# Kernel optimization log

Hardware: AMD Instinct MI355X
Metric: run time of the kernel (lower is better)

The kernel has to match this reference:

```python
import jax, jax.numpy as jnp
import numpy as np

B, S, D = 2, 2048, 1024
H = 16
HD = D // H

def setup_inputs() -> dict:
    key = jax.random.key(0)
    ks = jax.random.split(key, 6)
    sc = 0.02
    return {
        'x': jax.random.normal(ks[0], (B, S, D), jnp.float32),
        'Wq': jax.random.normal(ks[1], (D, D), jnp.float32) * sc,
        'Wk': jax.random.normal(ks[2], (D, D), jnp.float32) * sc,
        'Wv': jax.random.normal(ks[3], (D, D), jnp.float32) * sc,
        'Wo': jax.random.normal(ks[4], (D, D), jnp.float32) * sc,
        'bo': jnp.zeros((D,), jnp.float32),
    }

def reference(x, Wq, Wk, Wv, Wo, bo):
    b, s, d_in = x.shape
    # torch Linear: y = x @ W.T
    q = jnp.einsum('bsd,ed->bse', x, Wq)
    k = jnp.einsum('bsd,ed->bse', x, Wk)
    v = jnp.einsum('bsd,ed->bse', x, Wv)
    # [b, h, s, hd]
    q = q.reshape(b, s, H, HD).transpose(0, 2, 1, 3)
    k = k.reshape(b, s, H, HD).transpose(0, 2, 1, 3)
    v = v.reshape(b, s, H, HD).transpose(0, 2, 1, 3)
    # NOTE: original divides by sqrt(d_out), not sqrt(head_dim)
    scores = jnp.einsum('bhqd,bhkd->bhqk', q, k) / jnp.sqrt(jnp.float32(D))
    causal = jnp.tril(jnp.ones((s, s), dtype=bool))  # True = keep
    scores = jnp.where(causal[None, None], scores, -jnp.inf)
    attn = jax.nn.softmax(scores, axis=-1)
    ctx = jnp.einsum('bhqk,bhkd->bhqd', attn, v)
    ctx = ctx.transpose(0, 2, 1, 3).reshape(b, s, D)
    return jnp.einsum('bsd,ed->bse', ctx, Wo) + bo
```

## Files before the change

### kernel.cpp

```cpp
#include <hip/hip_runtime.h>
#include <hip/hip_bf16.h>
#include <stdint.h>

typedef unsigned short u16;
typedef __attribute__((ext_vector_type(8))) short short8;
typedef __attribute__((ext_vector_type(4))) float f32x4;
typedef __attribute__((ext_vector_type(16))) float f32x16;
typedef __attribute__((ext_vector_type(4))) u16 u16x4;

#define NB 2
#define NS 2048
#define ND 1024
#define NH 16
#define NM 4096

#define QSCALE 0.045084220f

#if __has_builtin(__builtin_amdgcn_exp2f)
#define EXP2(x) __builtin_amdgcn_exp2f(x)
#else
__device__ __forceinline__ float __exp2_asm(float x){
  float r;
  asm("v_exp_f32 %0, %1" : "=v"(r) : "v"(x));
  return r;
}
#define EXP2(x) __exp2_asm(x)
#endif
#if __has_builtin(__builtin_amdgcn_rcpf)
#define RCP(x) __builtin_amdgcn_rcpf(x)
#else
#define RCP(x) (1.0f / (x))
#endif

__device__ __forceinline__ u16 f2bf(float f){
  union { float f; unsigned u; } v; v.f = f;
  unsigned r = v.u + 0x7fff + ((v.u >> 16) & 1);
  return (u16)(r >> 16);
}

__device__ __forceinline__ unsigned cvtpk(float lo, float hi){
  unsigned r;
  asm("v_cvt_pk_bf16_f32 %0, %1, %2" : "=v"(r) : "v"(lo), "v"(hi));
  return r;
}

__device__ __forceinline__ void pl32swap(unsigned &e, unsigned &o){
  asm("v_permlane32_swap_b32 %0, %1" : "+v"(e), "+v"(o));
}

__device__ __forceinline__ void gload_lds16(const u16* g, u16* l){
  __builtin_amdgcn_global_load_lds(
      (const __attribute__((address_space(1))) unsigned int*)g,
      (__attribute__((address_space(3))) unsigned int*)l, 16, 0, 0);
}

__device__ __forceinline__ f32x16 mfma32(short8 a, short8 b, f32x16 c){
  return __builtin_amdgcn_mfma_f32_32x32x16_bf16(a, b, c, 0, 0, 0);
}

__global__ void cvt_all(const float* __restrict__ x,
                        const float* __restrict__ wq, const float* __restrict__ wk,
                        const float* __restrict__ wv, const float* __restrict__ wo,
                        u16* __restrict__ xb, u16* __restrict__ wqb, u16* __restrict__ wkb,
                        u16* __restrict__ wvb, u16* __restrict__ wob){
  int ib = blockIdx.x;
  const float* s; u16* d; int off;
  if (ib < 4096){ s = x; d = xb; off = ib; }
  else {
    int t = ib - 4096, sel = t >> 10;
    off = t & 1023;
    s = (sel == 0) ? wq : (sel == 1) ? wk : (sel == 2) ? wv : wo;
    d = (sel == 0) ? wqb : (sel == 1) ? wkb : (sel == 2) ? wvb : wob;
  }
  int i = (off * 256 + threadIdx.x) * 4;
  float4 v = *(const float4*)(s + i);
  u16x4 pk = { f2bf(v.x), f2bf(v.y), f2bf(v.z), f2bf(v.w) };
  *(u16x4*)(d + i) = pk;
}

__device__ __forceinline__ void gemm_core(
    const u16* __restrict__ A, const u16* __restrict__ W,
    int m0, int n0, u16* lsA, u16* lsB, f32x4 acc[4][4])
{
  const int tid = threadIdx.x;
  const int l   = tid & 63;
  const int wr  = (tid >> 7) & 1;
  const int wc  = (tid >> 6) & 1;
  const int lr  = l & 15;
  const int lkb = (l >> 4) << 4;
  const int sr  = tid >> 3;
  const int scb = (tid & 7) << 4;

  for (int kt = 0; kt < 16; ++kt){
    const int k0 = kt << 6;
    #pragma unroll
    for (int i = 0; i < 4; ++i){
      int r   = (i << 5) + sr;
      int cbs = scb ^ ((r & 7) << 4);
      gload_lds16(&A[(size_t)(m0 + r) * ND + k0 + (cbs >> 1)], &lsA[r * 64 + (scb >> 1)]);
      gload_lds16(&W[(size_t)(n0 + r) * ND + k0 + (cbs >> 1)], &lsB[r * 64 + (scb >> 1)]);
    }
    __syncthreads();

    short8 af[4][2], bf[4][2];
    #pragma unroll
    for (int m16 = 0; m16 < 4; ++m16){
      int r  = (wr << 6) + (m16 << 4) + lr;
      int rx = (r & 7) << 4;
      #pragma unroll
      for (int ks = 0; ks < 2; ++ks){
        int off = r * 128 + (((ks << 6) + lkb) ^ rx);
        af[m16][ks] = *(const short8*)((const char*)lsA + off);
      }
    }
    #pragma unroll
    for (int n16 = 0; n16 < 4; ++n16){
      int r  = (wc << 6) + (n16 << 4) + lr;
      int rx = (r & 7) << 4;
      #pragma unroll
      for (int ks = 0; ks < 2; ++ks){
        int off = r * 128 + (((ks << 6) + lkb) ^ rx);
        bf[n16][ks] = *(const short8*)((const char*)lsB + off);
      }
    }
    #pragma unroll
    for (int m16 = 0; m16 < 4; ++m16)
      #pragma unroll
      for (int n16 = 0; n16 < 4; ++n16){
        acc[m16][n16] = __builtin_amdgcn_mfma_f32_16x16x32_bf16(af[m16][0], bf[n16][0], acc[m16][n16], 0, 0, 0);
        acc[m16][n16] = __builtin_amdgcn_mfma_f32_16x16x32_bf16(af[m16][1], bf[n16][1], acc[m16][n16], 0, 0, 0);
      }
    __syncthreads();
  }
}

__global__ __launch_bounds__(256) void gemm_qkv(
    const u16* __restrict__ xb,
    const u16* __restrict__ Wqb, const u16* __restrict__ Wkb, const u16* __restrict__ Wvb,
    u16* __restrict__ Qo, u16* __restrict__ Ko, u16* __restrict__ Vt)
{
  __shared__ u16 lsA[128*64];
  __shared__ u16 lsB[128*64];
  const int z = blockIdx.z;
  const u16* W = (z == 0) ? Wqb : (z == 1) ? Wkb : Wvb;
  const int m0 = blockIdx.x << 7, n0 = blockIdx.y << 7;
  f32x4 acc[4][4] = {};
  gemm_core(xb, W, m0, n0, lsA, lsB, acc);

  const int l  = threadIdx.x & 63;
  const int wr = (threadIdx.x >> 7) & 1, wc = (threadIdx.x >> 6) & 1;
  const int rb = m0 + (wr << 6) + ((l >> 4) << 2);
  const int cb = n0 + (wc << 6) + (l & 15);

  if (z < 2){
    const float sc = (z == 0) ? QSCALE : 1.0f;
    u16* C = (z == 0) ? Qo : Ko;
    #pragma unroll
    for (int m16 = 0; m16 < 4; ++m16)
      #pragma unroll
      for (int n16 = 0; n16 < 4; ++n16)
        #pragma unroll
        for (int r = 0; r < 4; ++r)
          C[(size_t)(rb + (m16 << 4) + r) * ND + cb + (n16 << 4)] = f2bf(acc[m16][n16][r] * sc);
  } else {
    #pragma unroll
    for (int m16 = 0; m16 < 4; ++m16){
      int srow = rb + (m16 << 4);
      int bi = srow >> 11, s = srow & 2047;
      #pragma unroll
      for (int n16 = 0; n16 < 4; ++n16){
        int col = cb + (n16 << 4);
        u16x4 pk = { f2bf(acc[m16][n16][0]), f2bf(acc[m16][n16][1]),
                     f2bf(acc[m16][n16][2]), f2bf(acc[m16][n16][3]) };
        *(u16x4*)&Vt[((size_t)(bi * 16 + (col >> 6)) * 64 + (col & 63)) * 2048 + s] = pk;
      }
    }
  }
}

__global__ __launch_bounds__(256) void gemm_out(
    const u16* __restrict__ ctxb, const u16* __restrict__ Wob,
    const float* __restrict__ bo, float* __restrict__ out)
{
  __shared__ u16 lsA[64*64];
  __shared__ u16 lsB[128*64];
  const int m0 = blockIdx.x << 6, n0 = blockIdx.y << 7;
  const int tid = threadIdx.x;
  const int l = tid & 63;
  const int w = tid >> 6;
  const int lr = l & 15;
  const int lkb = (l >> 4) << 4;
  const int rl = tid >> 3, ch = tid & 7;

  f32x4 acc[4][2] = {};

  for (int kt = 0; kt < 16; ++kt){
    const int k0 = kt << 6;
    #pragma unroll
    for (int k = 0; k < 2; ++k){
      int rr = rl + (k << 5);
      int cs = ch ^ (rr & 7);
      gload_lds16(&ctxb[(size_t)(m0 + rr) * ND + k0 + cs * 8], &lsA[rr * 64 + ch * 8]);
    }
    #pragma unroll
    for (int k = 0; k < 4; ++k){
      int rr = rl + (k << 5);
      int cs = ch ^ (rr & 7);
      gload_lds16(&Wob[(size_t)(n0 + rr) * ND + k0 + cs * 8], &lsB[rr * 64 + ch * 8]);
    }
    __syncthreads();

    short8 af[4][2], bf[2][2];
    #pragma unroll
    for (int m16 = 0; m16 < 4; ++m16){
      int r  = (m16 << 4) + lr;
      int rx = (r & 7) << 4;
      #pragma unroll
      for (int ks = 0; ks < 2; ++ks)
        af[m16][ks] = *(const short8*)((const char*)lsA + r * 128 + (((ks << 6) + lkb) ^ rx));
    }
    #pragma unroll
    for (int n16 = 0; n16 < 2; ++n16){
      int r  = (w << 5) + (n16 << 4) + lr;
      int rx = (r & 7) << 4;
      #pragma unroll
      for (int ks = 0; ks < 2; ++ks)
        bf[n16][ks] = *(const short8*)((const char*)lsB + r * 128 + (((ks << 6) + lkb) ^ rx));
    }
    #pragma unroll
    for (int m16 = 0; m16 < 4; ++m16)
      #pragma unroll
      for (int n16 = 0; n16 < 2; ++n16){
        acc[m16][n16] = __builtin_amdgcn_mfma_f32_16x16x32_bf16(af[m16][0], bf[n16][0], acc[m16][n16], 0, 0, 0);
        acc[m16][n16] = __builtin_amdgcn_mfma_f32_16x16x32_bf16(af[m16][1], bf[n16][1], acc[m16][n16], 0, 0, 0);
      }
    __syncthreads();
  }

  const int rb = m0 + ((l >> 4) << 2);
  const int cb = n0 + (w << 5) + lr;
  #pragma unroll
  for (int m16 = 0; m16 < 4; ++m16)
    #pragma unroll
    for (int n16 = 0; n16 < 2; ++n16)
      #pragma unroll
      for (int r = 0; r < 4; ++r){
        int col = cb + (n16 << 4);
        out[(size_t)(rb + (m16 << 4) + r) * ND + col] = acc[m16][n16][r] + bo[col];
      }
}

__device__ __forceinline__ void stage_tile(const u16* src, int srcStride, u16* lds, int tid){
  const int rl = tid >> 3;
  const int ch = tid & 7;
  const int cs = ch ^ (rl & 7);
  gload_lds16(&src[(size_t)rl * srcStride + cs * 8],        &lds[rl * 64 + ch * 8]);
  gload_lds16(&src[(size_t)(rl + 32) * srcStride + cs * 8], &lds[(rl + 32) * 64 + ch * 8]);
}

__device__ __forceinline__ void qk_tile(const u16* lsKt, const short8 qf[4],
                                        int q5, int hi, f32x16 &s0, f32x16 &s1){
  const char* Kc = (const char*)lsKt;
  const int swz = q5 & 7;
  f32x16 a = {}, b = {};
  __builtin_amdgcn_s_setprio(1);
  #pragma unroll
  for (int ks = 0; ks < 4; ++ks){
    int c0 = ((2 * ks + hi) ^ swz) << 4;
    short8 k0 = *(const short8*)(Kc + q5 * 128 + c0);
    short8 k1 = *(const short8*)(Kc + (q5 + 32) * 128 + c0);
    a = mfma32(k0, qf[ks], a);
    b = mfma32(k1, qf[ks], b);
  }
  __builtin_amdgcn_s_setprio(0);
  s0 = a; s1 = b;
}

__device__ __forceinline__ void sm_pv(f32x16 s0, f32x16 s1, const u16* lsVt,
                                      int t, int qb, int qgl, int q5, int hi,
                                      float &m_r, float &l_r, f32x16 &accA, f32x16 &accB){
  if (t * 64 + 63 > qb){
    #pragma unroll
    for (int r = 0; r < 16; ++r){
      int kl = t * 64 + (r & 3) + 8 * (r >> 2) + 4 * hi;
      if (kl > qgl)      s0[r] = -3e38f;
      if (kl + 32 > qgl) s1[r] = -3e38f;
    }
  }
  float mx[16];
  #pragma unroll
  for (int r = 0; r < 16; ++r) mx[r] = fmaxf(s0[r], s1[r]);
  #pragma unroll
  for (int stp = 8; stp > 0; stp >>= 1)
    #pragma unroll
    for (int r = 0; r < stp; ++r) mx[r] = fmaxf(mx[r], mx[r + stp]);
  float pm = fmaxf(mx[0], __shfl_xor(mx[0], 32));

  if (__any(pm > m_r + 8.f)){
    float mn = fmaxf(m_r, pm);
    float e  = EXP2(m_r - mn);
    m_r = mn; l_r *= e;
    #pragma unroll
    for (int r = 0; r < 16; ++r){ accA[r] *= e; accB[r] *= e; }
  }

  #pragma unroll
  for (int r = 0; r < 16; ++r){
    s0[r] = EXP2(s0[r] - m_r);
    s1[r] = EXP2(s1[r] - m_r);
  }
  float sm[16];
  #pragma unroll
  for (int r = 0; r < 16; ++r) sm[r] = s0[r] + s1[r];
  #pragma unroll
  for (int stp = 8; stp > 0; stp >>= 1)
    #pragma unroll
    for (int r = 0; r < stp; ++r) sm[r] += sm[r + stp];
  l_r += sm[0] + __shfl_xor(sm[0], 32);

  unsigned pw[2][4][2];
  #pragma unroll
  for (int g = 0; g < 4; ++g){
    pw[0][g][0] = cvtpk(s0[4*g],     s0[4*g + 1]);
    pw[0][g][1] = cvtpk(s0[4*g + 2], s0[4*g + 3]);
    pw[1][g][0] = cvtpk(s1[4*g],     s1[4*g + 1]);
    pw[1][g][1] = cvtpk(s1[4*g + 2], s1[4*g + 3]);
  }
  #pragma unroll
  for (int m = 0; m < 2; ++m)
    #pragma unroll
    for (int kp = 0; kp < 2; ++kp)
      #pragma unroll
      for (int i = 0; i < 2; ++i)
        pl32swap(pw[m][2*kp][i], pw[m][2*kp + 1][i]);

  const char* Vc = (const char*)lsVt;
  const int swz = q5 & 7;
  __builtin_amdgcn_s_setprio(1);
  #pragma unroll
  for (int ks = 0; ks < 4; ++ks){
    const int m = ks >> 1, kp = ks & 1;
    union { unsigned u[4]; short8 s8; } pa;
    pa.u[0] = pw[m][2*kp][0];
    pa.u[1] = pw[m][2*kp][1];
    pa.u[2] = pw[m][2*kp + 1][0];
    pa.u[3] = pw[m][2*kp + 1][1];
    int c0 = ((2 * ks + hi) ^ swz) << 4;
    short8 v0 = *(const short8*)(Vc + q5 * 128 + c0);
    short8 v1 = *(const short8*)(Vc + (q5 + 32) * 128 + c0);
    accA = mfma32(pa.s8, v0, accA);
    accB = mfma32(pa.s8, v1, accB);
  }
  __builtin_amdgcn_s_setprio(0);
}

#define SUBITER(T, SC0, SC1, SN0, SN1)                                            \
  {                                                                               \
    const int t_ = (T);                                                           \
    if (t_ + 3 <= tb){                                                            \
      stage_tile(&Kb0[(size_t)(t_ + 3) * 64 * ND], ND, lsK[(t_ + 3) & 3], tid);   \
      stage_tile(&Vb0[(t_ + 3) * 64],              NS, lsV[(t_ + 3) & 3], tid);   \
    }                                                                             \
    if (t_ + 1 <= nc) qk_tile(lsK[(t_ + 1) & 3], qf, q5, hi, SN0, SN1);           \
    if (t_ <= nc)     sm_pv(SC0, SC1, lsV[t_ & 3], t_, qb, qgl, q5, hi,           \
                            m_r, l_r, accA, accB);                                \
    if (t_ + 3 <= tb) asm volatile("s_waitcnt vmcnt(4)" ::: "memory");            \
    else              asm volatile("s_waitcnt vmcnt(0)" ::: "memory");            \
    __builtin_amdgcn_sched_barrier(0);                                            \
    __builtin_amdgcn_s_barrier();                                                 \
    __builtin_amdgcn_sched_barrier(0);                                            \
  }

__global__ __launch_bounds__(256, 2) void attn_kernel(
    const u16* __restrict__ Q, const u16* __restrict__ K,
    const u16* __restrict__ Vt, u16* __restrict__ ctx)
{
  __shared__ __align__(16) u16 lsK[4][64*64];
  __shared__ __align__(16) u16 lsV[4][64*64];

  const int bid = blockIdx.x;
  const int xcd = bid & 7;
  const int j   = bid >> 3;
  const int strm = (j & 31) >> 3;
  const int idx  = j & 7;
  const int st   = (j < 32) ? (15 - idx) : idx;
  const int bh   = xcd + 8 * strm;
  const int b = bh >> 4, h = bh & 15;
  const int tid = threadIdx.x;
  const int l = tid & 63, w = tid >> 6;
  const int q5 = l & 31, hi = l >> 5;
  const int qb   = st * 128 + w * 32;
  const int qgl  = qb + q5;
  const int nc   = (qb + 31) >> 6;
  const int tb   = 2 * st + 1;

  const u16* Kb0 = &K[(size_t)(b * NS) * ND + h * 64];
  const u16* Vb0 = &Vt[(size_t)bh * 64 * NS];

  short8 qf[4];
  {
    const u16* Qrow = &Q[(size_t)(b * NS + qgl) * ND + h * 64 + hi * 8];
    #pragma unroll
    for (int ks = 0; ks < 4; ++ks)
      qf[ks] = *(const short8*)&Qrow[ks * 16];
  }

  float m_r = -3e38f, l_r = 0.f;
  f32x16 accA = {}, accB = {};
  f32x16 sA0, sA1, sB0, sB1;

  stage_tile(Kb0, ND, lsK[0], tid);
  stage_tile(Vb0, NS, lsV[0], tid);
  stage_tile(&Kb0[(size_t)64 * ND], ND, lsK[1], tid);
  stage_tile(&Vb0[64],              NS, lsV[1], tid);
  if (2 <= tb){
    stage_tile(&Kb0[(size_t)128 * ND], ND, lsK[2], tid);
    stage_tile(&Vb0[128],              NS, lsV[2], tid);
    asm volatile("s_waitcnt vmcnt(4)" ::: "memory");
  } else {
    asm volatile("s_waitcnt vmcnt(0)" ::: "memory");
  }
  __builtin_amdgcn_sched_barrier(0);
  __builtin_amdgcn_s_barrier();
  __builtin_amdgcn_sched_barrier(0);
  qk_tile(lsK[0], qf, q5, hi, sA0, sA1);

  #pragma unroll 1
  for (int t = 0; t <= tb; t += 2){
    SUBITER(t,     sA0, sA1, sB0, sB1);
    SUBITER(t + 1, sB0, sB1, sA0, sA1);
  }

  float inv = RCP(l_r);
  #pragma unroll
  for (int r = 0; r < 16; ++r){
    int qrow = (r & 3) + 8 * (r >> 2) + 4 * hi;
    float iv = __shfl(inv, (l & 32) | qrow, 64);
    u16* crow = &ctx[(size_t)(b * NS + qb + qrow) * ND + h * 64 + q5];
    crow[0]  = f2bf(accA[r] * iv);
    crow[32] = f2bf(accB[r] * iv);
  }
}

extern "C" void kernel_launch(void* const* d_in, const int* in_sizes, int n_in,
                              void* d_out, int out_size, void* d_ws, size_t ws_size,
                              hipStream_t stream)
{
  const float* x  = (const float*)d_in[0];
  const float* Wq = (const float*)d_in[1];
  const float* Wk = (const float*)d_in[2];
  const float* Wv = (const float*)d_in[3];
  const float* Wo = (const float*)d_in[4];
  const float* bo = (const float*)d_in[5];
  float* out = (float*)d_out;
  char* ws = (char*)d_ws;

  u16* xb  = (u16*)(ws);
  u16* Wqb = (u16*)(ws + (8u  << 20));
  u16* Wkb = (u16*)(ws + (10u << 20));
  u16* Wvb = (u16*)(ws + (12u << 20));
  u16* Wob = (u16*)(ws + (14u << 20));
  u16* Qb  = (u16*)(ws + (16u << 20));
  u16* Kb  = (u16*)(ws + (24u << 20));
  u16* Vtb = (u16*)(ws + (32u << 20));
  u16* Cb  = (u16*)(ws + (40u << 20));

  cvt_all<<<8192, 256, 0, stream>>>(x, Wq, Wk, Wv, Wo, xb, Wqb, Wkb, Wvb, Wob);

  gemm_qkv<<<dim3(32, 8, 3), 256, 0, stream>>>(xb, Wqb, Wkb, Wvb, Qb, Kb, Vtb);
  attn_kernel<<<512, 256, 0, stream>>>(Qb, Kb, Vtb, Cb);
  gemm_out<<<dim3(64, 8), 256, 0, stream>>>(Cb, Wob, bo, out);
}
```

Measured before the change: 117.4 us.

## Load V fragments directly from global into registers instead of LDS staging

V^T tiles are no longer staged through a 4-deep LDS ring buffer. Each wave now reads its PV MFMA operands straight from global memory at the start of each sub-iteration, and the vmcnt thresholds are adjusted to count only the K staging loads. This halves LDS use and removes the V stage/read traffic through shared memory. The cost is that the V loads are issued in the same iteration they are consumed, so global latency may be exposed, and the 64x64 V tile is read redundantly by each of the 4 waves.

```diff
diff --git a/kernel.cpp b/kernel.cpp
--- a/kernel.cpp
+++ b/kernel.cpp
@@ -276,8 +276,8 @@
   s0 = a; s1 = b;
 }
 
-__device__ __forceinline__ void sm_pv(f32x16 s0, f32x16 s1, const u16* lsVt,
-                                      int t, int qb, int qgl, int q5, int hi,
+__device__ __forceinline__ void sm_pv(f32x16 s0, f32x16 s1, const short8 vf[4][2],
+                                      int t, int qb, int qgl, int hi,
                                       float &m_r, float &l_r, f32x16 &accA, f32x16 &accB){
   if (t * 64 + 63 > qb){
     #pragma unroll
@@ -334,8 +334,6 @@
       for (int i = 0; i < 2; ++i)
         pl32swap(pw[m][2*kp][i], pw[m][2*kp + 1][i]);
 
-  const char* Vc = (const char*)lsVt;
-  const int swz = q5 & 7;
   __builtin_amdgcn_s_setprio(1);
   #pragma unroll
   for (int ks = 0; ks < 4; ++ks){
@@ -345,11 +343,8 @@
     pa.u[1] = pw[m][2*kp][1];
     pa.u[2] = pw[m][2*kp + 1][0];
     pa.u[3] = pw[m][2*kp + 1][1];
-    int c0 = ((2 * ks + hi) ^ swz) << 4;
-    short8 v0 = *(const short8*)(Vc + q5 * 128 + c0);
-    short8 v1 = *(const short8*)(Vc + (q5 + 32) * 128 + c0);
-    accA = mfma32(pa.s8, v0, accA);
-    accB = mfma32(pa.s8, v1, accB);
+    accA = mfma32(pa.s8, vf[ks][0], accA);
+    accB = mfma32(pa.s8, vf[ks][1], accB);
   }
   __builtin_amdgcn_s_setprio(0);
 }
@@ -357,14 +352,21 @@
 #define SUBITER(T, SC0, SC1, SN0, SN1)                                            \
   {                                                                               \
     const int t_ = (T);                                                           \
-    if (t_ + 3 <= tb){                                                            \
+    short8 vf[4][2];                                                              \
+    if (t_ <= nc){                                                                \
+      const u16* vb = Vb0 + (size_t)t_ * 64;                                      \
+      _Pragma("unroll")                                                           \
+      for (int ks = 0; ks < 4; ++ks){                                             \
+        vf[ks][0] = *(const short8*)&vb[(size_t)q5 * NS + (2 * ks + hi) * 8];     \
+        vf[ks][1] = *(const short8*)&vb[(size_t)(q5 + 32) * NS + (2 * ks + hi) * 8]; \
+      }                                                                           \
+    }                                                                             \
+    if (t_ + 3 <= tb)                                                             \
       stage_tile(&Kb0[(size_t)(t_ + 3) * 64 * ND], ND, lsK[(t_ + 3) & 3], tid);   \
-      stage_tile(&Vb0[(t_ + 3) * 64],              NS, lsV[(t_ + 3) & 3], tid);   \
-    }                                                                             \
     if (t_ + 1 <= nc) qk_tile(lsK[(t_ + 1) & 3], qf, q5, hi, SN0, SN1);           \
-    if (t_ <= nc)     sm_pv(SC0, SC1, lsV[t_ & 3], t_, qb, qgl, q5, hi,           \
+    if (t_ <= nc)     sm_pv(SC0, SC1, vf, t_, qb, qgl, hi,                        \
                             m_r, l_r, accA, accB);                                \
-    if (t_ + 3 <= tb) asm volatile("s_waitcnt vmcnt(4)" ::: "memory");            \
+    if (t_ + 3 <= tb) asm volatile("s_waitcnt vmcnt(2)" ::: "memory");            \
     else              asm volatile("s_waitcnt vmcnt(0)" ::: "memory");            \
     __builtin_amdgcn_sched_barrier(0);                                            \
     __builtin_amdgcn_s_barrier();                                                 \
@@ -376,7 +378,6 @@
     const u16* __restrict__ Vt, u16* __restrict__ ctx)
 {
   __shared__ __align__(16) u16 lsK[4][64*64];
-  __shared__ __align__(16) u16 lsV[4][64*64];
 
   const int bid = blockIdx.x;
   const int xcd = bid & 7;
@@ -410,13 +411,10 @@
   f32x16 sA0, sA1, sB0, sB1;
 
   stage_tile(Kb0, ND, lsK[0], tid);
-  stage_tile(Vb0, NS, lsV[0], tid);
   stage_tile(&Kb0[(size_t)64 * ND], ND, lsK[1], tid);
-  stage_tile(&Vb0[64],              NS, lsV[1], tid);
   if (2 <= tb){
     stage_tile(&Kb0[(size_t)128 * ND], ND, lsK[2], tid);
-    stage_tile(&Vb0[128],              NS, lsV[2], tid);
-    asm volatile("s_waitcnt vmcnt(4)" ::: "memory");
+    asm volatile("s_waitcnt vmcnt(2)" ::: "memory");
   } else {
     asm volatile("s_waitcnt vmcnt(0)" ::: "memory");
   }
```

Result: no change. 118.8 us (+1.2%).
